# Optimization experiments

Measured on AMD Instinct MI355X. Metric: run time of the kernel, lower is better.

The kernel has to match this reference:

```python
import jax, jax.numpy as jnp
import numpy as np

L, B, E, H = 1024, 8, 1024, 16


def setup_inputs() -> dict:
    key = jax.random.key(0)
    k1, k2, k3, k4, k5 = jax.random.split(key, 5)
    scale = 1.0 / np.sqrt(E)
    return {
        "x": jax.random.normal(k1, (L, B, E), dtype=jnp.float32),
        "in_proj_weight": jax.random.normal(k2, (3 * E, E), dtype=jnp.float32) * scale,
        "in_proj_bias": jax.random.normal(k3, (3 * E,), dtype=jnp.float32) * 0.01,
        "out_proj_weight": jax.random.normal(k4, (E, E), dtype=jnp.float32) * scale,
        "out_proj_bias": jax.random.normal(k5, (E,), dtype=jnp.float32) * 0.01,
        "num_heads": H,
    }


def reference(x, in_proj_weight, in_proj_bias, out_proj_weight, out_proj_bias, num_heads):
    # x: [L, B, E] (tgt_len, batch, embed_dim), self-attention path of
    # multi_head_attention_func (no masks, no bias_k/v, no add_zero_attn,
    # dropout_p=0 / eval mode).
    Lq, Bq, Eq = x.shape
    hd = Eq // num_heads
    scaling = float(hd) ** -0.5
    # fused qkv projection: linear(x, in_proj_weight, in_proj_bias).chunk(3)
    qkv = x @ in_proj_weight.T + in_proj_bias  # [L, B, 3E]
    q, k, v = jnp.split(qkv, 3, axis=-1)
    q = q * scaling
    def to_heads(t):  # [L, B, E] -> [B*H, L, hd]
        return t.reshape(Lq, Bq * num_heads, hd).transpose(1, 0, 2)
    q, k, v = to_heads(q), to_heads(k), to_heads(v)
    # explicit QK^T -> softmax -> PV (naive attention, as in the source)
    scores = jnp.einsum('bqd,bkd->bqk', q, k)      # [B*H, L, L]
    attn = jax.nn.softmax(scores, axis=-1)
    out = jnp.einsum('bqk,bkd->bqd', attn, v)      # [B*H, L, hd]
    out = out.transpose(1, 0, 2).reshape(Lq, Bq, Eq)
    out = out @ out_proj_weight.T + out_proj_bias  # [L, B, E]
    return out
```

## Files before the change

kernel.cpp:

```cpp
#include <hip/hip_runtime.h>

#define L_DIM 1024
#define B_DIM 8
#define E_DIM 1024
#define H_DIM 16
#define HD 64
#define BH_DIM (B_DIM * H_DIM)

typedef float f32x4 __attribute__((ext_vector_type(4)));
typedef _Float16 f16_t;
typedef f16_t f16x4 __attribute__((ext_vector_type(4)));
typedef f16_t f16x8 __attribute__((ext_vector_type(8)));

static __device__ __forceinline__ void gld16(const void* g, void* l) {
  __builtin_amdgcn_global_load_lds(
      (const __attribute__((address_space(1))) unsigned int*)g,
      (__attribute__((address_space(3))) unsigned int*)l, 16, 0, 0);
}

__global__ __launch_bounds__(256) void convert_f16(
    const float* __restrict__ x, const float* __restrict__ wi,
    const float* __restrict__ wo, f16_t* __restrict__ x16,
    f16_t* __restrict__ wi16, f16_t* __restrict__ wo16) {
  const int NX = (L_DIM * B_DIM * E_DIM) / 4;
  const int NWI = (3 * E_DIM * E_DIM) / 4;
  const int NWO = (E_DIM * E_DIM) / 4;
  const int total = NX + NWI + NWO;
  for (int i = blockIdx.x * blockDim.x + threadIdx.x; i < total;
       i += gridDim.x * blockDim.x) {
    const float4* src; f16_t* dst; int j;
    if (i < NX)            { src = (const float4*)x;  dst = x16;  j = i; }
    else if (i < NX + NWI) { src = (const float4*)wi; dst = wi16; j = i - NX; }
    else                   { src = (const float4*)wo; dst = wo16; j = i - NX - NWI; }
    const float4 v = src[j];
    f16x4 h = {(f16_t)v.x, (f16_t)v.y, (f16_t)v.z, (f16_t)v.w};
    *(f16x4*)(dst + (size_t)j * 4) = h;
  }
}


#define GQ_FENCE asm volatile("" ::: "memory")
#define GQ_BARRIER do { GQ_FENCE; __builtin_amdgcn_s_barrier(); GQ_FENCE; } while (0)
#define VMW(n) asm volatile("s_waitcnt vmcnt(" #n ")" ::: "memory")

static __device__ __forceinline__ const f16x8* fp16frag(
    const f16_t* tile, int r, int ks, int quad, int l16) {
  const int bo = (r * 128 + ks * 64 + quad * 16) ^ ((l16 & 7) << 4);
  return (const f16x8*)((const char*)tile + bo);
}

__global__ __launch_bounds__(256, 2) void gemm_qkv(
    const f16_t* __restrict__ A, const f16_t* __restrict__ B,
    const float* __restrict__ bias, f16_t* __restrict__ Oq,
    f16_t* __restrict__ Ok, f16_t* __restrict__ Ov) {
  constexpr int K = 1024;
  __shared__ __align__(16) f16_t As[2 * 8192];
  __shared__ __align__(16) f16_t Bs[2 * 8192];

  const int tid = threadIdx.x;
  const int lane = tid & 63;
  const int w = tid >> 6;
  const int wm = (w & 1) * 64;
  const int wn = (w >> 1) * 64;
  const int quad = lane >> 4;
  const int l16 = lane & 15;

  const int bid = blockIdx.x;
  const int xcd = bid & 7;
  const int idx = bid >> 3;
  const int tm = xcd * 8 + (idx & 7);
  const int tn = idx >> 3;
  const int m0 = tm * 128;
  const int n0 = tn * 128;

  const int r8 = tid >> 3;
  const int gsw = (tid & 7) ^ (r8 & 7);
  const f16_t* Abase = A + (size_t)(m0 + r8) * K + gsw * 8;
  const f16_t* Bbase = B + (size_t)(n0 + r8) * K + gsw * 8;

#define STAGE(kt, d) do {                                                    \
    _Pragma("unroll") for (int s_ = 0; s_ < 4; ++s_)                         \
      gld16(Abase + (size_t)s_ * 32 * K + (kt) * 64,                         \
            &As[(d) * 8192 + s_ * 2048 + tid * 8]);                          \
    _Pragma("unroll") for (int s_ = 0; s_ < 4; ++s_)                         \
      gld16(Bbase + (size_t)s_ * 32 * K + (kt) * 64,                         \
            &Bs[(d) * 8192 + s_ * 2048 + tid * 8]);                          \
  } while (0)

  f32x4 acc[4][4] = {};

  STAGE(0, 0);
  STAGE(1, 1);

#pragma unroll
  for (int t = 0; t < 16; ++t) {
    const int d = t & 1;
    VMW(8);
    GQ_BARRIER;

    f16x8 af[4][2], bf[4][2];
#pragma unroll
    for (int i = 0; i < 4; ++i)
#pragma unroll
      for (int ks = 0; ks < 2; ++ks) {
        af[i][ks] = *fp16frag(&As[d * 8192], wm + i * 16 + l16, ks, quad, l16);
        bf[i][ks] = *fp16frag(&Bs[d * 8192], wn + i * 16 + l16, ks, quad, l16);
      }

    __builtin_amdgcn_s_setprio(1);
#pragma unroll
    for (int i = 0; i < 4; ++i)
#pragma unroll
      for (int j = 0; j < 4; ++j)
#pragma unroll
        for (int ks = 0; ks < 2; ++ks)
          acc[i][j] = __builtin_amdgcn_mfma_f32_16x16x32_f16(
              af[i][ks], bf[j][ks], acc[i][j], 0, 0, 0);
    __builtin_amdgcn_s_setprio(0);

    GQ_BARRIER;
    const int kt2 = (t + 2 < 16) ? t + 2 : 15;
    STAGE(kt2, d);
  }

#pragma unroll
  for (int i = 0; i < 4; ++i) {
    const int mbase = m0 + wm + i * 16 + quad * 4;
#pragma unroll
    for (int c = 0; c < 4; ++c) {
      const int n = n0 + wn + c * 16 + l16;
      const float bv = bias[n];
      const int chunk = n >> 10;
      const int e = n & 1023;
      const int h = e >> 6;
      const int dd = e & 63;
#pragma unroll
      for (int r = 0; r < 4; ++r) {
        const int m = mbase + r;
        const int l = m >> 3, b = m & 7;
        const size_t idxo = ((size_t)(b * H_DIM + h) * L_DIM + l) * HD + dd;
        const float val = acc[i][c][r] + bv;
        if (chunk == 0)      Oq[idxo] = (f16_t)(val * 0.125f);
        else if (chunk == 1) Ok[idxo] = (f16_t)val;
        else                 Ov[idxo] = (f16_t)val;
      }
    }
  }
#undef STAGE
}

template <int MODE>
__global__ __launch_bounds__(256, 2) void gemm_f16(
    const f16_t* __restrict__ A, const f16_t* __restrict__ B,
    const float* __restrict__ bias, void* __restrict__ O0v,
    void* __restrict__ O1v, void* __restrict__ O2v) {
  constexpr int K = 1024;
  __shared__ __align__(16) f16_t As[128 * 32];
  __shared__ __align__(16) f16_t Bs[128 * 32];

  const int tid = threadIdx.x;
  const int lane = tid & 63;
  const int wave = tid >> 6;
  const int wm = (wave & 1) * 64;
  const int wn = (wave >> 1) * 64;
  const int quad = lane >> 4;
  const int l16 = lane & 15;
  const int m0 = blockIdx.y * 128;
  const int n0 = blockIdx.x * 128;

  const int cr = tid >> 2;
  const int cc = (tid & 3) * 8;

  f32x4 acc[4][4] = {};

  for (int k0 = 0; k0 < K; k0 += 32) {
    __syncthreads();
    gld16(A + (size_t)(m0 + cr) * K + k0 + cc,      As + tid * 8);
    gld16(A + (size_t)(m0 + 64 + cr) * K + k0 + cc, As + 2048 + tid * 8);
    gld16(B + (size_t)(n0 + cr) * K + k0 + cc,      Bs + tid * 8);
    gld16(B + (size_t)(n0 + 64 + cr) * K + k0 + cc, Bs + 2048 + tid * 8);
    __syncthreads();

    f16x8 af[4], bfr[4];
#pragma unroll
    for (int t = 0; t < 4; ++t) {
      af[t]  = *(const f16x8*)&As[(wm + t * 16 + l16) * 32 + quad * 8];
      bfr[t] = *(const f16x8*)&Bs[(wn + t * 16 + l16) * 32 + quad * 8];
    }
#pragma unroll
    for (int i = 0; i < 4; ++i)
#pragma unroll
      for (int j = 0; j < 4; ++j)
        acc[i][j] = __builtin_amdgcn_mfma_f32_16x16x32_f16(af[i], bfr[j], acc[i][j], 0, 0, 0);
  }

#pragma unroll
  for (int i = 0; i < 4; ++i) {
    const int mbase = m0 + wm + i * 16 + quad * 4;
#pragma unroll
    for (int j = 0; j < 4; ++j) {
      const int n = n0 + wn + j * 16 + l16;
      const float bv = bias[n];
      if (MODE == 0) {
        f16_t* O0 = (f16_t*)O0v; f16_t* O1 = (f16_t*)O1v; f16_t* O2 = (f16_t*)O2v;
        const int chunk = n >> 10;
        const int e = n & 1023;
        const int h = e >> 6;
        const int d = e & 63;
#pragma unroll
        for (int r = 0; r < 4; ++r) {
          const int m = mbase + r;
          const int l = m >> 3, b = m & 7;
          const size_t idx = ((size_t)(b * H_DIM + h) * L_DIM + l) * HD + d;
          const float val = acc[i][j][r] + bv;
          if (chunk == 0)      O0[idx] = (f16_t)(val * 0.125f);
          else if (chunk == 1) O1[idx] = (f16_t)val;
          else                 O2[idx] = (f16_t)val;
        }
      } else {
        float* O0 = (float*)O0v;
#pragma unroll
        for (int r = 0; r < 4; ++r) {
          const int m = mbase + r;
          O0[(size_t)m * E_DIM + n] = acc[i][j][r] + bv;
        }
      }
    }
  }
}

__global__ __launch_bounds__(256, 2) void attn_f16(
    const f16_t* __restrict__ Q, const f16_t* __restrict__ K,
    const f16_t* __restrict__ V, f16_t* __restrict__ O) {
  constexpr int KSTR = 70;
  __shared__ __align__(16) f16_t Ks[2][64 * KSTR];
  __shared__ __align__(16) f16_t Vs[2][64 * KSTR];
  __shared__ float Ls[4][64];

  const int tid = threadIdx.x;
  const int lane = tid & 63;
  const int w = tid >> 6;
  const int quad = lane >> 4;
  const int l16 = lane & 15;
  const int bh = blockIdx.y;
  const int q0 = blockIdx.x * 256 + w * 64;

  const f16_t* Qb = Q + (size_t)bh * L_DIM * HD;
  const f16_t* Kb = K + (size_t)bh * L_DIM * HD;
  const f16_t* Vb = V + (size_t)bh * L_DIM * HD;

  f16x8 qf[4][2];
#pragma unroll
  for (int nt = 0; nt < 4; ++nt)
#pragma unroll
    for (int kc = 0; kc < 2; ++kc)
      qf[nt][kc] = *(const f16x8*)(Qb + (size_t)(q0 + nt * 16 + l16) * HD + kc * 32 + quad * 8);

  f32x4 oacc[4][4] = {};
  float rsum[4] = {0.0f, 0.0f, 0.0f, 0.0f};

  const int sr = tid >> 3;
  const int sc8 = (tid & 7) * 8;
  const int va = tid & 31;
  const int vg = tid >> 5;
  const int rA = (l16 >> 2) * 8 + (l16 & 3);

  f16x8 kreg[2];
  unsigned int vd[8];

#define LOADKV(kt) do {                                                      \
    _Pragma("unroll") for (int rr_ = 0; rr_ < 2; ++rr_)                      \
      kreg[rr_] = *(const f16x8*)(Kb +                                       \
          (size_t)((kt) * 64 + sr + rr_ * 32) * HD + sc8);                   \
    const f16_t* vp_ = Vb + (size_t)((kt) * 64 + vg * 8) * HD + 2 * va;      \
    _Pragma("unroll") for (int i_ = 0; i_ < 8; ++i_)                         \
      vd[i_] = *(const unsigned int*)(vp_ + (size_t)i_ * HD);                \
  } while (0)

#define WRITEKV(nb) do {                                                     \
    _Pragma("unroll") for (int rr_ = 0; rr_ < 2; ++rr_)                      \
      *(f16x8*)&Ks[nb][(sr + rr_ * 32) * KSTR + sc8] = kreg[rr_];            \
    union { unsigned int u[4]; f16x8 v; } lo_, hi_;                          \
    _Pragma("unroll") for (int i_ = 0; i_ < 4; ++i_) {                       \
      lo_.u[i_] = (vd[2 * i_] & 0xffffu) | (vd[2 * i_ + 1] << 16);           \
      hi_.u[i_] = (vd[2 * i_] >> 16) | (vd[2 * i_ + 1] & 0xffff0000u);       \
    }                                                                        \
    *(f16x8*)&Vs[nb][(2 * va) * KSTR + vg * 8] = lo_.v;                      \
    *(f16x8*)&Vs[nb][(2 * va + 1) * KSTR + vg * 8] = hi_.v;                  \
  } while (0)

#define ATTN_SYNC do {                                                       \
    GQ_FENCE;                                                                \
    asm volatile("s_waitcnt lgkmcnt(0)" ::: "memory");                       \
    __builtin_amdgcn_s_barrier();                                            \
    GQ_FENCE;                                                                \
  } while (0)

#define ATTN_COMPUTE(nb) do {                                                \
    _Pragma("unroll") for (int c = 0; c < 2; ++c) {                          \
      f32x4 scv[2][4] = {};                                                  \
      __builtin_amdgcn_s_setprio(1);                                         \
      _Pragma("unroll") for (int h = 0; h < 2; ++h) {                        \
        const int row = c * 32 + h * 4 + rA;                                 \
        _Pragma("unroll") for (int kc = 0; kc < 2; ++kc) {                   \
          const f16x8 ka = *(const f16x8*)&Ks[nb][row * KSTR + kc * 32 + quad * 8]; \
          _Pragma("unroll") for (int nt = 0; nt < 4; ++nt)                   \
            scv[h][nt] = __builtin_amdgcn_mfma_f32_16x16x32_f16(             \
                ka, qf[nt][kc], scv[h][nt], 0, 0, 0);                        \
        }                                                                    \
      }                                                                      \
      __builtin_amdgcn_s_setprio(0);                                         \
      f16x8 pa[4];                                                           \
      _Pragma("unroll") for (int nt = 0; nt < 4; ++nt)                       \
        _Pragma("unroll") for (int h = 0; h < 2; ++h)                        \
          _Pragma("unroll") for (int r = 0; r < 4; ++r) {                    \
            const float e = __expf(scv[h][nt][r]);                           \
            rsum[nt] += e;                                                   \
            pa[nt][h * 4 + r] = (f16_t)e;                                    \
          }                                                                  \
      __builtin_amdgcn_s_setprio(1);                                         \
      _Pragma("unroll") for (int nd = 0; nd < 4; ++nd) {                     \
        const f16x8 vb = *(const f16x8*)&Vs[nb][(nd * 16 + l16) * KSTR + c * 32 + quad * 8]; \
        _Pragma("unroll") for (int nt = 0; nt < 4; ++nt)                     \
          oacc[nt][nd] = __builtin_amdgcn_mfma_f32_16x16x32_f16(             \
              pa[nt], vb, oacc[nt][nd], 0, 0, 0);                            \
      }                                                                      \
      __builtin_amdgcn_s_setprio(0);                                         \
    }                                                                        \
  } while (0)

  LOADKV(0);
  WRITEKV(0);
  LOADKV(1);
  ATTN_SYNC;

  for (int kt = 0; kt < 14; kt += 2) {
    ATTN_COMPUTE(0);
    WRITEKV(1);
    LOADKV(kt + 2);
    ATTN_SYNC;
    ATTN_COMPUTE(1);
    WRITEKV(0);
    LOADKV(kt + 3);
    ATTN_SYNC;
  }
  ATTN_COMPUTE(0);
  WRITEKV(1);
  ATTN_SYNC;
  ATTN_COMPUTE(1);

#undef LOADKV
#undef WRITEKV
#undef ATTN_SYNC
#undef ATTN_COMPUTE

#pragma unroll
  for (int nt = 0; nt < 4; ++nt) {
    float rs = rsum[nt];
    rs += __shfl_xor(rs, 16); rs += __shfl_xor(rs, 32);
    if (quad == 0) Ls[w][nt * 16 + l16] = rs;
  }
  asm volatile("s_waitcnt lgkmcnt(0)" ::: "memory");

  const int b = bh >> 4;
  const int h = bh & 15;
#pragma unroll
  for (int nt = 0; nt < 4; ++nt)
#pragma unroll
    for (int r = 0; r < 4; ++r) {
      const int ql = nt * 16 + quad * 4 + r;
      const float inv = 1.0f / Ls[w][ql];
      const int qrow = q0 + ql;
#pragma unroll
      for (int nd = 0; nd < 4; ++nd) {
        const int d = nd * 16 + l16;
        O[((size_t)qrow * B_DIM + b) * E_DIM + h * HD + d] = (f16_t)(oacc[nt][nd][r] * inv);
      }
    }
}

extern "C" void kernel_launch(void* const* d_in, const int* in_sizes, int n_in,
                              void* d_out, int out_size, void* d_ws, size_t ws_size,
                              hipStream_t stream) {
  const float* x     = (const float*)d_in[0];
  const float* w_in  = (const float*)d_in[1];
  const float* b_in  = (const float*)d_in[2];
  const float* w_out = (const float*)d_in[3];
  const float* b_out = (const float*)d_in[4];

  const size_t TS = (size_t)BH_DIM * L_DIM * HD;
  f16_t* q16  = (f16_t*)d_ws;
  f16_t* k16  = q16 + TS;
  f16_t* v16  = k16 + TS;
  f16_t* x16  = v16 + TS;
  f16_t* wi16 = x16 + TS;
  f16_t* wo16 = wi16 + (size_t)3 * E_DIM * E_DIM;
  f16_t* ao16 = x16;

  convert_f16<<<4096, 256, 0, stream>>>(x, w_in, w_out, x16, wi16, wo16);
  gemm_qkv<<<1536, 256, 0, stream>>>(x16, wi16, b_in, q16, k16, v16);
  attn_f16<<<dim3(4, 128), 256, 0, stream>>>(q16, k16, v16, ao16);
  gemm_f16<1><<<dim3(8, 64), 256, 0, stream>>>(ao16, wo16, b_out, d_out, nullptr, nullptr);
}
```

Baseline: 227.0 us.

## Rewrite output projection GEMM with double-buffered K=64 pipeline and XCD-aware tile mapping

Replaces the generic templated GEMM used for the output projection with a dedicated kernel. It stages 64-wide K tiles into double-buffered LDS with XOR-swizzled global-to-LDS loads and waits on vmcnt instead of full syncs, so the next tile's loads overlap the current MFMAs. It also raises wave priority around the MFMA block and remaps the 1D grid so that tiles sharing A rows land on the same XCD for L2 reuse. The cost is doubled LDS use, which may lower occupancy, and reliance on helper macros (VMW, GQ_BARRIER, fp16frag) assumed to be defined elsewhere.

```diff
diff --git a/kernel.cpp b/kernel.cpp
--- a/kernel.cpp
+++ b/kernel.cpp
@@ -149,84 +149,94 @@
 #undef STAGE
 }
 
-template <int MODE>
-__global__ __launch_bounds__(256, 2) void gemm_f16(
+__global__ __launch_bounds__(256, 2) void gemm_out(
     const f16_t* __restrict__ A, const f16_t* __restrict__ B,
-    const float* __restrict__ bias, void* __restrict__ O0v,
-    void* __restrict__ O1v, void* __restrict__ O2v) {
+    const float* __restrict__ bias, float* __restrict__ O) {
   constexpr int K = 1024;
-  __shared__ __align__(16) f16_t As[128 * 32];
-  __shared__ __align__(16) f16_t Bs[128 * 32];
+  __shared__ __align__(16) f16_t As[2 * 8192];
+  __shared__ __align__(16) f16_t Bs[2 * 8192];
 
   const int tid = threadIdx.x;
   const int lane = tid & 63;
-  const int wave = tid >> 6;
-  const int wm = (wave & 1) * 64;
-  const int wn = (wave >> 1) * 64;
+  const int w = tid >> 6;
+  const int wm = (w & 1) * 64;
+  const int wn = (w >> 1) * 64;
   const int quad = lane >> 4;
   const int l16 = lane & 15;
-  const int m0 = blockIdx.y * 128;
-  const int n0 = blockIdx.x * 128;
-
-  const int cr = tid >> 2;
-  const int cc = (tid & 3) * 8;
+
+  const int bid = blockIdx.x;
+  const int xcd = bid & 7;
+  const int idx = bid >> 3;
+  const int tm = xcd * 8 + (idx & 7);
+  const int tn = idx >> 3;
+  const int m0 = tm * 128;
+  const int n0 = tn * 128;
+
+  const int r8 = tid >> 3;
+  const int gsw = (tid & 7) ^ (r8 & 7);
+  const f16_t* Abase = A + (size_t)(m0 + r8) * K + gsw * 8;
+  const f16_t* Bbase = B + (size_t)(n0 + r8) * K + gsw * 8;
+
+#define STAGE(kt, d) do {                                                    \
+    _Pragma("unroll") for (int s_ = 0; s_ < 4; ++s_)                         \
+      gld16(Abase + (size_t)s_ * 32 * K + (kt) * 64,                         \
+            &As[(d) * 8192 + s_ * 2048 + tid * 8]);                          \
+    _Pragma("unroll") for (int s_ = 0; s_ < 4; ++s_)                         \
+      gld16(Bbase + (size_t)s_ * 32 * K + (kt) * 64,                         \
+            &Bs[(d) * 8192 + s_ * 2048 + tid * 8]);                          \
+  } while (0)
 
   f32x4 acc[4][4] = {};
 
-  for (int k0 = 0; k0 < K; k0 += 32) {
-    __syncthreads();
-    gld16(A + (size_t)(m0 + cr) * K + k0 + cc,      As + tid * 8);
-    gld16(A + (size_t)(m0 + 64 + cr) * K + k0 + cc, As + 2048 + tid * 8);
-    gld16(B + (size_t)(n0 + cr) * K + k0 + cc,      Bs + tid * 8);
-    gld16(B + (size_t)(n0 + 64 + cr) * K + k0 + cc, Bs + 2048 + tid * 8);
-    __syncthreads();
-
-    f16x8 af[4], bfr[4];
-#pragma unroll
-    for (int t = 0; t < 4; ++t) {
-      af[t]  = *(const f16x8*)&As[(wm + t * 16 + l16) * 32 + quad * 8];
-      bfr[t] = *(const f16x8*)&Bs[(wn + t * 16 + l16) * 32 + quad * 8];
-    }
+  STAGE(0, 0);
+  STAGE(1, 1);
+
+#pragma unroll
+  for (int t = 0; t < 16; ++t) {
+    const int d = t & 1;
+    VMW(8);
+    GQ_BARRIER;
+
+    f16x8 af[4][2], bf[4][2];
 #pragma unroll
     for (int i = 0; i < 4; ++i)
 #pragma unroll
+      for (int ks = 0; ks < 2; ++ks) {
+        af[i][ks] = *fp16frag(&As[d * 8192], wm + i * 16 + l16, ks, quad, l16);
+        bf[i][ks] = *fp16frag(&Bs[d * 8192], wn + i * 16 + l16, ks, quad, l16);
+      }
+
+    __builtin_amdgcn_s_setprio(1);
+#pragma unroll
+    for (int i = 0; i < 4; ++i)
+#pragma unroll
       for (int j = 0; j < 4; ++j)
-        acc[i][j] = __builtin_amdgcn_mfma_f32_16x16x32_f16(af[i], bfr[j], acc[i][j], 0, 0, 0);
+#pragma unroll
+        for (int ks = 0; ks < 2; ++ks)
+          acc[i][j] = __builtin_amdgcn_mfma_f32_16x16x32_f16(
+              af[i][ks], bf[j][ks], acc[i][j], 0, 0, 0);
+    __builtin_amdgcn_s_setprio(0);
+
+    GQ_BARRIER;
+    const int kt2 = (t + 2 < 16) ? t + 2 : 15;
+    STAGE(kt2, d);
   }
 
 #pragma unroll
   for (int i = 0; i < 4; ++i) {
     const int mbase = m0 + wm + i * 16 + quad * 4;
 #pragma unroll
-    for (int j = 0; j < 4; ++j) {
-      const int n = n0 + wn + j * 16 + l16;
+    for (int c = 0; c < 4; ++c) {
+      const int n = n0 + wn + c * 16 + l16;
       const float bv = bias[n];
-      if (MODE == 0) {
-        f16_t* O0 = (f16_t*)O0v; f16_t* O1 = (f16_t*)O1v; f16_t* O2 = (f16_t*)O2v;
-        const int chunk = n >> 10;
-        const int e = n & 1023;
-        const int h = e >> 6;
-        const int d = e & 63;
-#pragma unroll
-        for (int r = 0; r < 4; ++r) {
-          const int m = mbase + r;
-          const int l = m >> 3, b = m & 7;
-          const size_t idx = ((size_t)(b * H_DIM + h) * L_DIM + l) * HD + d;
-          const float val = acc[i][j][r] + bv;
-          if (chunk == 0)      O0[idx] = (f16_t)(val * 0.125f);
-          else if (chunk == 1) O1[idx] = (f16_t)val;
-          else                 O2[idx] = (f16_t)val;
-        }
-      } else {
-        float* O0 = (float*)O0v;
-#pragma unroll
-        for (int r = 0; r < 4; ++r) {
-          const int m = mbase + r;
-          O0[(size_t)m * E_DIM + n] = acc[i][j][r] + bv;
-        }
+#pragma unroll
+      for (int r = 0; r < 4; ++r) {
+        const int m = mbase + r;
+        O[(size_t)m * E_DIM + n] = acc[i][c][r] + bv;
       }
     }
   }
+#undef STAGE
 }
 
 __global__ __launch_bounds__(256, 2) void attn_f16(
@@ -400,5 +410,5 @@
   convert_f16<<<4096, 256, 0, stream>>>(x, w_in, w_out, x16, wi16, wo16);
   gemm_qkv<<<1536, 256, 0, stream>>>(x16, wi16, b_in, q16, k16, v16);
   attn_f16<<<dim3(4, 128), 256, 0, stream>>>(q16, k16, v16, ao16);
-  gemm_f16<1><<<dim3(8, 64), 256, 0, stream>>>(ao16, wo16, b_out, d_out, nullptr, nullptr);
-}
+  gemm_out<<<512, 256, 0, stream>>>(ao16, wo16, b_out, (float*)d_out);
+}
```

After: 225.2 us. No clear change (-0.8%).
